# Kernel optimization log

Measured on AMD Instinct MI355X. Metric: run time of the kernel, lower is better.

Reference implementation:

```python
import jax, jax.numpy as jnp
import numpy as np

D_MODEL = 1024
NUM_HEADS = 16
DEPTH = D_MODEL // NUM_HEADS
B, S = 4, 2048


def setup_inputs() -> dict:
    key = jax.random.key(0)
    ks = jax.random.split(key, 11)
    sc = 1.0 / np.sqrt(D_MODEL)
    return {
        "query": jax.random.normal(ks[0], (B, S, D_MODEL), jnp.float32),
        "key_": jax.random.normal(ks[1], (B, S, D_MODEL), jnp.float32),
        "value": jax.random.normal(ks[2], (B, S, D_MODEL), jnp.float32),
        # torch Linear: y = x @ W.T + b, W shape [out, in]
        "Wq": jax.random.normal(ks[3], (D_MODEL, D_MODEL), jnp.float32) * sc,
        "bq": jax.random.normal(ks[4], (D_MODEL,), jnp.float32) * sc,
        "Wk": jax.random.normal(ks[5], (D_MODEL, D_MODEL), jnp.float32) * sc,
        "bk": jax.random.normal(ks[6], (D_MODEL,), jnp.float32) * sc,
        "Wv": jax.random.normal(ks[7], (D_MODEL, D_MODEL), jnp.float32) * sc,
        "bv": jax.random.normal(ks[8], (D_MODEL,), jnp.float32) * sc,
        "Wo": jax.random.normal(ks[9], (D_MODEL, D_MODEL), jnp.float32) * sc,
        "bo": jax.random.normal(ks[10], (D_MODEL,), jnp.float32) * sc,
    }


def _split_heads(x):
    # [B,S,D] -> [B,H,S,depth]
    b, s, _ = x.shape
    return x.reshape(b, s, NUM_HEADS, DEPTH).transpose(0, 2, 1, 3)


def reference(query, key_, value, Wq, bq, Wk, bk, Wv, bv, Wo, bo):
    Q = _split_heads(query @ Wq.T + bq)
    K = _split_heads(key_ @ Wk.T + bk)
    V = _split_heads(value @ Wv.T + bv)
    scale = 1.0 / jnp.sqrt(jnp.float32(DEPTH))
    scores = jnp.einsum("bhqd,bhkd->bhqk", Q, K) * scale  # [B,H,S,S]
    attention_weights = jax.nn.softmax(scores, axis=-1)
    out = jnp.einsum("bhqk,bhkd->bhqd", attention_weights, V)
    out = out.transpose(0, 2, 1, 3).reshape(query.shape[0], -1, D_MODEL)
    out = out @ Wo.T + bo
    return out, attention_weights
```

## Files before the change

kernel.cpp:

```cpp
#include <hip/hip_runtime.h>

#define NHEAD 16
#define SEQ 2048
#define DMODEL 1024
#define BB 4
#define MROWS (BB*SEQ)
#define NBH (BB*NHEAD)
#define NT (SEQ/32)

typedef float f32x4 __attribute__((ext_vector_type(4)));
typedef _Float16 f16x8 __attribute__((ext_vector_type(8)));
typedef _Float16 f16x4 __attribute__((ext_vector_type(4)));

static __device__ __forceinline__ f32x4 mfma16(f16x8 a, f16x8 b, f32x4 c) {
  return __builtin_amdgcn_mfma_f32_16x16x32_f16(a, b, c, 0, 0, 0);
}

static __device__ __forceinline__ void gload_lds16(const unsigned short* g, unsigned short* l) {
  __builtin_amdgcn_global_load_lds(
      (const __attribute__((address_space(1))) unsigned int*)g,
      (__attribute__((address_space(3))) unsigned int*)l, 16, 0, 0);
}

static __device__ __forceinline__ ushort4 cvt4(float4 x) {
  ushort4 h;
  h.x = __builtin_bit_cast(unsigned short, (_Float16)x.x);
  h.y = __builtin_bit_cast(unsigned short, (_Float16)x.y);
  h.z = __builtin_bit_cast(unsigned short, (_Float16)x.z);
  h.w = __builtin_bit_cast(unsigned short, (_Float16)x.w);
  return h;
}

__global__ __launch_bounds__(256)
void round3_f16(const float* __restrict__ q, const float* __restrict__ k,
                const float* __restrict__ v,
                unsigned short* __restrict__ oq, unsigned short* __restrict__ ok,
                unsigned short* __restrict__ ov, int n4)
{
  const float* src = (blockIdx.y == 0) ? q : (blockIdx.y == 1) ? k : v;
  unsigned short* dst = (blockIdx.y == 0) ? oq : (blockIdx.y == 1) ? ok : ov;
  int i = blockIdx.x*256 + threadIdx.x;
  const int stride = gridDim.x*256;
  for (; i < n4; i += stride)
    ((ushort4*)dst)[i] = cvt4(((const float4*)src)[i]);
}

__global__ __launch_bounds__(256)
void round_w4(const float* __restrict__ w0, const float* __restrict__ w1,
              const float* __restrict__ w2, const float* __restrict__ w3,
              unsigned short* __restrict__ o0, unsigned short* __restrict__ o1,
              unsigned short* __restrict__ o2, unsigned short* __restrict__ o3, int n4)
{
  const float* src = (blockIdx.y == 0) ? w0 : (blockIdx.y == 1) ? w1
                   : (blockIdx.y == 2) ? w2 : w3;
  unsigned short* dst = (blockIdx.y == 0) ? o0 : (blockIdx.y == 1) ? o1
                      : (blockIdx.y == 2) ? o2 : o3;
  int i = blockIdx.x*256 + threadIdx.x;
  const int stride = gridDim.x*256;
  for (; i < n4; i += stride)
    ((ushort4*)dst)[i] = cvt4(((const float4*)src)[i]);
}

static __device__ __forceinline__ void stage_proj(
    unsigned short* ab, unsigned short* bb,
    const unsigned short* __restrict__ Xf, const unsigned short* __restrict__ Wf,
    int m0, int n0, int k0, int tid)
{
#pragma unroll
  for (int r = 0; r < 2; ++r) {
    const int gi = r*256 + tid;
    const int row = gi >> 2, c = gi & 3;
    const int lg = c ^ ((row >> 1) & 3);
    gload_lds16(Xf + (size_t)(m0+row)*DMODEL + k0 + lg*8,
                ab + r*2048 + (tid & 0xC0)*8);
  }
#pragma unroll
  for (int r = 0; r < 2; ++r) {
    const int gi = r*256 + tid;
    const int row = gi >> 2, c = gi & 3;
    const int lg = c ^ ((row >> 1) & 3);
    gload_lds16(Wf + (size_t)(n0+row)*DMODEL + k0 + lg*8,
                bb + r*2048 + (tid & 0xC0)*8);
  }
}

template<int MODE>
__global__ __launch_bounds__(256, 2)
void proj_gemm(const unsigned short* __restrict__ Xf, const unsigned short* __restrict__ Wf,
               const float* __restrict__ bias, float oscale,
               unsigned short* __restrict__ o16, float* __restrict__ o_f32)
{
  __shared__ unsigned short As[2][128][32];
  __shared__ unsigned short Bs[2][128][32];
  const int tid  = threadIdx.x;
  const int wid  = tid >> 6, lane = tid & 63;
  const int g    = lane >> 4, r16 = lane & 15;
  const int id   = blockIdx.y*64 + blockIdx.x;
  const int xcd  = id & 7, slot = id >> 3;
  const int m0   = (xcd*8 + (slot & 7)) * 128;
  const int n0   = (slot >> 3) * 128;
  const int wr   = wid >> 1, wc = wid & 1;

  f32x4 acc[4][4] = {};

  stage_proj(&As[0][0][0], &Bs[0][0][0], Xf, Wf, m0, n0, 0, tid);
  asm volatile("s_waitcnt vmcnt(0)" ::: "memory");
  __builtin_amdgcn_s_barrier();

  for (int kt = 0; kt < 32; ++kt) {
    const int cur = kt & 1;
    if (kt < 31)
      stage_proj(&As[cur^1][0][0], &Bs[cur^1][0][0], Xf, Wf, m0, n0, (kt+1)*32, tid);

    const unsigned short (*Asb)[32] = As[cur];
    const unsigned short (*Bsb)[32] = Bs[cur];
    f16x8 a[4], b[4];
#pragma unroll
    for (int t = 0; t < 4; ++t) {
      const int ar = wr*64 + t*16 + r16;
      a[t] = *(const f16x8*)((const char*)&Asb[ar][0] + ((g ^ ((ar >> 1) & 3)) << 4));
      const int br = wc*64 + t*16 + r16;
      b[t] = *(const f16x8*)((const char*)&Bsb[br][0] + ((g ^ ((br >> 1) & 3)) << 4));
    }
    __builtin_amdgcn_s_setprio(1);
#pragma unroll
    for (int mt = 0; mt < 4; ++mt)
#pragma unroll
      for (int nt = 0; nt < 4; ++nt)
        acc[mt][nt] = mfma16(a[mt], b[nt], acc[mt][nt]);
    __builtin_amdgcn_s_setprio(0);

    if (kt < 31) {
      asm volatile("s_waitcnt vmcnt(0)" ::: "memory");
      __builtin_amdgcn_s_barrier();
    }
  }

#pragma unroll
  for (int nt = 0; nt < 4; ++nt) {
    const int n  = n0 + wc*64 + nt*16 + r16;
    const float bn = bias[n];
#pragma unroll
    for (int mt = 0; mt < 4; ++mt) {
      const int mb = m0 + wr*64 + mt*16 + g*4;
      if (MODE == 0) {
#pragma unroll
        for (int j = 0; j < 4; ++j) {
          const int m = mb + j;
          const int bt = m >> 11, s = m & (SEQ-1);
          const int hh = n >> 6,  d = n & 63;
          o16[(((size_t)(bt*NHEAD + hh)*SEQ + s) << 6) + d] =
              __builtin_bit_cast(unsigned short, (_Float16)((acc[mt][nt][j] + bn) * oscale));
        }
      } else if (MODE == 1) {
        const int bt = mb >> 11, sb = mb & (SEQ-1);
        const int hh = n >> 6,  d = n & 63;
        ushort4 v;
        v.x = __builtin_bit_cast(unsigned short, (_Float16)(acc[mt][nt][0] + bn));
        v.y = __builtin_bit_cast(unsigned short, (_Float16)(acc[mt][nt][1] + bn));
        v.z = __builtin_bit_cast(unsigned short, (_Float16)(acc[mt][nt][2] + bn));
        v.w = __builtin_bit_cast(unsigned short, (_Float16)(acc[mt][nt][3] + bn));
        *(ushort4*)(o16 + ((size_t)(bt*NHEAD + hh)*64 + d)*SEQ + sb) = v;
      } else {
#pragma unroll
        for (int j = 0; j < 4; ++j)
          o_f32[(size_t)(mb + j)*DMODEL + n] = acc[mt][nt][j] + bn;
      }
    }
  }
}

static __device__ __forceinline__ void stage_k(unsigned short* dst,
    const unsigned short* __restrict__ Kf, size_t kbase, int k0, int tid)
{
  const int row = tid >> 3, c = tid & 7;
  const int sg = c ^ (row & 7);
  gload_lds16(Kf + kbase + (size_t)(k0+row)*64 + sg*8, dst + (tid & 0xC0)*8);
}

static __device__ __forceinline__ void stage_v(unsigned short* dst,
    const unsigned short* __restrict__ Vtg, int bh, int k0, int tid)
{
  const int row = tid >> 2, c = tid & 3;
  const int lg = c ^ ((row >> 1) & 3);
  gload_lds16(Vtg + ((size_t)bh*64 + row)*SEQ + k0 + lg*8, dst + (tid & 0xC0)*8);
}

__global__ __launch_bounds__(256, 5)
void attn_fused(const unsigned short* __restrict__ Qf, const unsigned short* __restrict__ Kf,
                const unsigned short* __restrict__ Vtg,
                float* __restrict__ wout, unsigned short* __restrict__ of16)
{
  __shared__ unsigned short Ks[3][32][64];
  __shared__ unsigned short Vs[3][64][32];
  __shared__ unsigned short PA[4][16][40];
  const int tid = threadIdx.x, wid = tid >> 6, lane = tid & 63;
  const int g = lane >> 4, r16 = lane & 15;
  const int id = blockIdx.y*32 + blockIdx.x;
  const int xcd = id & 7, slot = id >> 3;
  const int bh = (slot >> 5)*8 + xcd;
  const int bx = slot & 31;
  const int bt = bh >> 4, hh = bh & (NHEAD-1);
  const int s0 = bx*64 + wid*16;
  const size_t kbase = (size_t)bh*SEQ*64;

  const size_t qoff = ((size_t)bh*SEQ + s0 + r16)*64 + (size_t)g*8;
  const f16x8 qh0 = *(const f16x8*)(Qf + qoff);
  const f16x8 qh1 = *(const f16x8*)(Qf + qoff + 32);

  float lp = 0.f;
  stage_k(&Ks[0][0][0], Kf, kbase, 0, tid);
  stage_k(&Ks[1][0][0], Kf, kbase, 32, tid);
  asm volatile("s_waitcnt vmcnt(1)" ::: "memory");
  __builtin_amdgcn_s_barrier();
  {
    int cur = 0, nxt = 2;
    for (int kt = 0; kt < NT; ++kt) {
      const bool pf = kt < NT-2;
      if (pf) stage_k(&Ks[nxt][0][0], Kf, kbase, (kt+2)*32, tid);
#pragma unroll
      for (int sub = 0; sub < 2; ++sub) {
        const int krow = sub*16 + r16;
        const char* pk = (const char*)&Ks[cur][krow][0];
        const int sx = krow & 7;
        const f16x8 kh0 = *(const f16x8*)(pk + (((g    ) ^ sx) << 4));
        const f16x8 kh1 = *(const f16x8*)(pk + (((4 | g) ^ sx) << 4));
        f32x4 acc = {};
        __builtin_amdgcn_s_setprio(1);
        acc = mfma16(kh0, qh0, acc);
        acc = mfma16(kh1, qh1, acc);
        __builtin_amdgcn_s_setprio(0);
#pragma unroll
        for (int j = 0; j < 4; ++j) lp += __builtin_exp2f(acc[j]);
      }
      if (pf) { asm volatile("s_waitcnt vmcnt(1)" ::: "memory"); }
      else    { asm volatile("s_waitcnt vmcnt(0)" ::: "memory"); }
      __builtin_amdgcn_s_barrier();
      cur = (cur == 2) ? 0 : cur + 1;
      nxt = (nxt == 2) ? 0 : nxt + 1;
    }
  }
  lp += __shfl_xor(lp, 16);
  lp += __shfl_xor(lp, 32);
  const float li = 1.0f / lp;

  f32x4 acco[4] = {};
  char* paw = (char*)&PA[wid][0][0];

  stage_k(&Ks[0][0][0], Kf, kbase, 0, tid);
  stage_v(&Vs[0][0][0], Vtg, bh, 0, tid);
  stage_k(&Ks[1][0][0], Kf, kbase, 32, tid);
  stage_v(&Vs[1][0][0], Vtg, bh, 32, tid);
  asm volatile("s_waitcnt vmcnt(2)" ::: "memory");
  __builtin_amdgcn_s_barrier();
  {
    int cur = 0, nxt = 2;
    for (int kt = 0; kt < NT; ++kt) {
      if (kt < NT-2) {
        stage_k(&Ks[nxt][0][0], Kf, kbase, (kt+2)*32, tid);
        stage_v(&Vs[nxt][0][0], Vtg, bh, (kt+2)*32, tid);
      }
#pragma unroll
      for (int sub = 0; sub < 2; ++sub) {
        const int krow = sub*16 + r16;
        const char* pk = (const char*)&Ks[cur][krow][0];
        const int sx = krow & 7;
        const f16x8 kh0 = *(const f16x8*)(pk + (((g    ) ^ sx) << 4));
        const f16x8 kh1 = *(const f16x8*)(pk + (((4 | g) ^ sx) << 4));
        f32x4 acc = {};
        __builtin_amdgcn_s_setprio(1);
        acc = mfma16(kh0, qh0, acc);
        acc = mfma16(kh1, qh1, acc);
        __builtin_amdgcn_s_setprio(0);
        f32x4 w4;
        f16x4 p4;
#pragma unroll
        for (int j = 0; j < 4; ++j) {
          w4[j] = __builtin_exp2f(acc[j]) * li;
          p4[j] = (_Float16)w4[j];
        }
        float* wp = wout + ((size_t)bh*SEQ + s0 + r16)*SEQ + kt*32 + sub*16 + 4*g;
        __builtin_nontemporal_store(w4, (f32x4*)wp);
        *(f16x4*)(paw + r16*80 + ((((2*sub + (g >> 1)) ^ (r16 & 3)) << 4) | ((g & 1) << 3))) = p4;
      }
      asm volatile("s_waitcnt lgkmcnt(0)" ::: "memory");
      const f16x8 pa = *(const f16x8*)(paw + r16*80 + ((g ^ (r16 & 3)) << 4));
      __builtin_amdgcn_s_setprio(1);
#pragma unroll
      for (int nt = 0; nt < 4; ++nt) {
        const int vrow = nt*16 + r16;
        const f16x8 vv = *(const f16x8*)((const char*)&Vs[cur][vrow][0] +
                                         ((g ^ ((vrow >> 1) & 3)) << 4));
        acco[nt] = mfma16(pa, vv, acco[nt]);
      }
      __builtin_amdgcn_s_setprio(0);
      if (kt == 0) {
        asm volatile("s_waitcnt vmcnt(4)" ::: "memory"); __builtin_amdgcn_s_barrier();
      } else if (kt < NT-2) {
        asm volatile("s_waitcnt vmcnt(6)" ::: "memory"); __builtin_amdgcn_s_barrier();
      } else if (kt == NT-2) {
        asm volatile("s_waitcnt vmcnt(4)" ::: "memory"); __builtin_amdgcn_s_barrier();
      }
      cur = (cur == 2) ? 0 : cur + 1;
      nxt = (nxt == 2) ? 0 : nxt + 1;
    }
  }

#pragma unroll
  for (int nt = 0; nt < 4; ++nt)
#pragma unroll
    for (int j = 0; j < 4; ++j)
      of16[((size_t)bt*SEQ + s0 + 4*g + j)*DMODEL + hh*64 + nt*16 + r16] =
          __builtin_bit_cast(unsigned short, (_Float16)acco[nt][j]);
}

extern "C" void kernel_launch(void* const* d_in, const int* in_sizes, int n_in,
                              void* d_out, int out_size, void* d_ws, size_t ws_size,
                              hipStream_t stream)
{
  const float* query = (const float*)d_in[0];
  const float* key_  = (const float*)d_in[1];
  const float* value = (const float*)d_in[2];
  const float* Wq = (const float*)d_in[3];
  const float* bq = (const float*)d_in[4];
  const float* Wk = (const float*)d_in[5];
  const float* bk = (const float*)d_in[6];
  const float* Wv = (const float*)d_in[7];
  const float* bv = (const float*)d_in[8];
  const float* Wo = (const float*)d_in[9];
  const float* bo = (const float*)d_in[10];

  const size_t NE = (size_t)NBH * SEQ * 64;
  const size_t NW = (size_t)DMODEL * DMODEL;
  unsigned short* Xq16 = (unsigned short*)d_ws;
  unsigned short* Xk16 = Xq16 + NE;
  unsigned short* Xv16 = Xk16 + NE;
  unsigned short* Qf   = Xv16 + NE;
  unsigned short* Kf   = Qf + NE;
  unsigned short* Vt   = Kf + NE;
  unsigned short* Wq16 = Vt + NE;
  unsigned short* Wk16 = Wq16 + NW;
  unsigned short* Wv16 = Wk16 + NW;
  unsigned short* Wo16 = Wv16 + NW;
  unsigned short* Of   = Xq16;

  float* out0  = (float*)d_out;
  float* wattn = out0 + (size_t)MROWS * DMODEL;

  const int nX4 = MROWS*DMODEL/4, nW4 = DMODEL*DMODEL/4;
  const float QSCALE = 0.125f * 1.4426950408889634f;
  dim3 gg(64, 8);

  round3_f16<<<dim3(1024, 3), 256, 0, stream>>>(query, key_, value, Xq16, Xk16, Xv16, nX4);
  round_w4<<<dim3(256, 4), 256, 0, stream>>>(Wq, Wk, Wv, Wo, Wq16, Wk16, Wv16, Wo16, nW4);

  proj_gemm<0><<<gg, dim3(256), 0, stream>>>(Xq16, Wq16, bq, QSCALE, Qf, nullptr);
  proj_gemm<0><<<gg, dim3(256), 0, stream>>>(Xk16, Wk16, bk, 1.0f, Kf, nullptr);
  proj_gemm<1><<<gg, dim3(256), 0, stream>>>(Xv16, Wv16, bv, 1.0f, Vt, nullptr);

  attn_fused<<<dim3(32, NBH), dim3(256), 0, stream>>>(Qf, Kf, Vt, wattn, Of);

  proj_gemm<2><<<gg, dim3(256), 0, stream>>>(Of, Wo16, bo, 1.0f, nullptr, out0);
}
```

Baseline: 500.1 us.

## Merge QKV projections into one launch and double query rows per attention wave

The three Q/K/V projection GEMMs are merged into one launch with a z-dimension that selects operands, which removes two kernel launches and lets the three GEMMs share the GPU concurrently. The attention kernel now has each wave handle 32 query rows instead of 16, so each K/V tile loaded into LDS feeds twice as many MFMAs. The grid is halved to match, the P staging buffer is doubled, and the vmcnt waits are adjusted for the extra outstanding stores. In exchange it raises register pressure (launch bounds go from 5 to 4 blocks per SM) and leaves fewer blocks to balance load across the GPU.

```diff
diff --git a/kernel.cpp b/kernel.cpp
--- a/kernel.cpp
+++ b/kernel.cpp
@@ -84,11 +84,102 @@
   }
 }
 
-template<int MODE>
 __global__ __launch_bounds__(256, 2)
-void proj_gemm(const unsigned short* __restrict__ Xf, const unsigned short* __restrict__ Wf,
-               const float* __restrict__ bias, float oscale,
-               unsigned short* __restrict__ o16, float* __restrict__ o_f32)
+void proj_qkv(const unsigned short* __restrict__ Xq, const unsigned short* __restrict__ Xk,
+              const unsigned short* __restrict__ Xv,
+              const unsigned short* __restrict__ Wqm, const unsigned short* __restrict__ Wkm,
+              const unsigned short* __restrict__ Wvm,
+              const float* __restrict__ bq, const float* __restrict__ bk,
+              const float* __restrict__ bv, float qscale,
+              unsigned short* __restrict__ oQ, unsigned short* __restrict__ oK,
+              unsigned short* __restrict__ oV)
+{
+  __shared__ unsigned short As[2][128][32];
+  __shared__ unsigned short Bs[2][128][32];
+  const int z = blockIdx.z;
+  const unsigned short* Xf = (z == 0) ? Xq : (z == 1) ? Xk : Xv;
+  const unsigned short* Wf = (z == 0) ? Wqm : (z == 1) ? Wkm : Wvm;
+  const float* bias = (z == 0) ? bq : (z == 1) ? bk : bv;
+  unsigned short* o16 = (z == 0) ? oQ : (z == 1) ? oK : oV;
+  const float oscale = (z == 0) ? qscale : 1.0f;
+
+  const int tid  = threadIdx.x;
+  const int wid  = tid >> 6, lane = tid & 63;
+  const int g    = lane >> 4, r16 = lane & 15;
+  const int id   = blockIdx.y*64 + blockIdx.x;
+  const int xcd  = id & 7, slot = id >> 3;
+  const int m0   = (xcd*8 + (slot & 7)) * 128;
+  const int n0   = (slot >> 3) * 128;
+  const int wr   = wid >> 1, wc = wid & 1;
+
+  f32x4 acc[4][4] = {};
+
+  stage_proj(&As[0][0][0], &Bs[0][0][0], Xf, Wf, m0, n0, 0, tid);
+  asm volatile("s_waitcnt vmcnt(0)" ::: "memory");
+  __builtin_amdgcn_s_barrier();
+
+  for (int kt = 0; kt < 32; ++kt) {
+    const int cur = kt & 1;
+    if (kt < 31)
+      stage_proj(&As[cur^1][0][0], &Bs[cur^1][0][0], Xf, Wf, m0, n0, (kt+1)*32, tid);
+
+    const unsigned short (*Asb)[32] = As[cur];
+    const unsigned short (*Bsb)[32] = Bs[cur];
+    f16x8 a[4], b[4];
+#pragma unroll
+    for (int t = 0; t < 4; ++t) {
+      const int ar = wr*64 + t*16 + r16;
+      a[t] = *(const f16x8*)((const char*)&Asb[ar][0] + ((g ^ ((ar >> 1) & 3)) << 4));
+      const int br = wc*64 + t*16 + r16;
+      b[t] = *(const f16x8*)((const char*)&Bsb[br][0] + ((g ^ ((br >> 1) & 3)) << 4));
+    }
+    __builtin_amdgcn_s_setprio(1);
+#pragma unroll
+    for (int mt = 0; mt < 4; ++mt)
+#pragma unroll
+      for (int nt = 0; nt < 4; ++nt)
+        acc[mt][nt] = mfma16(a[mt], b[nt], acc[mt][nt]);
+    __builtin_amdgcn_s_setprio(0);
+
+    if (kt < 31) {
+      asm volatile("s_waitcnt vmcnt(0)" ::: "memory");
+      __builtin_amdgcn_s_barrier();
+    }
+  }
+
+#pragma unroll
+  for (int nt = 0; nt < 4; ++nt) {
+    const int n  = n0 + wc*64 + nt*16 + r16;
+    const float bn = bias[n];
+#pragma unroll
+    for (int mt = 0; mt < 4; ++mt) {
+      const int mb = m0 + wr*64 + mt*16 + g*4;
+      if (z < 2) {
+#pragma unroll
+        for (int j = 0; j < 4; ++j) {
+          const int m = mb + j;
+          const int bt = m >> 11, s = m & (SEQ-1);
+          const int hh = n >> 6,  d = n & 63;
+          o16[(((size_t)(bt*NHEAD + hh)*SEQ + s) << 6) + d] =
+              __builtin_bit_cast(unsigned short, (_Float16)((acc[mt][nt][j] + bn) * oscale));
+        }
+      } else {
+        const int bt = mb >> 11, sb = mb & (SEQ-1);
+        const int hh = n >> 6,  d = n & 63;
+        ushort4 v;
+        v.x = __builtin_bit_cast(unsigned short, (_Float16)(acc[mt][nt][0] + bn));
+        v.y = __builtin_bit_cast(unsigned short, (_Float16)(acc[mt][nt][1] + bn));
+        v.z = __builtin_bit_cast(unsigned short, (_Float16)(acc[mt][nt][2] + bn));
+        v.w = __builtin_bit_cast(unsigned short, (_Float16)(acc[mt][nt][3] + bn));
+        *(ushort4*)(o16 + ((size_t)(bt*NHEAD + hh)*64 + d)*SEQ + sb) = v;
+      }
+    }
+  }
+}
+
+__global__ __launch_bounds__(256, 2)
+void proj_o(const unsigned short* __restrict__ Xf, const unsigned short* __restrict__ Wf,
+            const float* __restrict__ bias, float* __restrict__ o_f32)
 {
   __shared__ unsigned short As[2][128][32];
   __shared__ unsigned short Bs[2][128][32];
@@ -143,29 +234,9 @@
 #pragma unroll
     for (int mt = 0; mt < 4; ++mt) {
       const int mb = m0 + wr*64 + mt*16 + g*4;
-      if (MODE == 0) {
-#pragma unroll
-        for (int j = 0; j < 4; ++j) {
-          const int m = mb + j;
-          const int bt = m >> 11, s = m & (SEQ-1);
-          const int hh = n >> 6,  d = n & 63;
-          o16[(((size_t)(bt*NHEAD + hh)*SEQ + s) << 6) + d] =
-              __builtin_bit_cast(unsigned short, (_Float16)((acc[mt][nt][j] + bn) * oscale));
-        }
-      } else if (MODE == 1) {
-        const int bt = mb >> 11, sb = mb & (SEQ-1);
-        const int hh = n >> 6,  d = n & 63;
-        ushort4 v;
-        v.x = __builtin_bit_cast(unsigned short, (_Float16)(acc[mt][nt][0] + bn));
-        v.y = __builtin_bit_cast(unsigned short, (_Float16)(acc[mt][nt][1] + bn));
-        v.z = __builtin_bit_cast(unsigned short, (_Float16)(acc[mt][nt][2] + bn));
-        v.w = __builtin_bit_cast(unsigned short, (_Float16)(acc[mt][nt][3] + bn));
-        *(ushort4*)(o16 + ((size_t)(bt*NHEAD + hh)*64 + d)*SEQ + sb) = v;
-      } else {
-#pragma unroll
-        for (int j = 0; j < 4; ++j)
-          o_f32[(size_t)(mb + j)*DMODEL + n] = acc[mt][nt][j] + bn;
-      }
+#pragma unroll
+      for (int j = 0; j < 4; ++j)
+        o_f32[(size_t)(mb + j)*DMODEL + n] = acc[mt][nt][j] + bn;
     }
   }
 }
@@ -186,29 +257,31 @@
   gload_lds16(Vtg + ((size_t)bh*64 + row)*SEQ + k0 + lg*8, dst + (tid & 0xC0)*8);
 }
 
-__global__ __launch_bounds__(256, 5)
+__global__ __launch_bounds__(256, 4)
 void attn_fused(const unsigned short* __restrict__ Qf, const unsigned short* __restrict__ Kf,
                 const unsigned short* __restrict__ Vtg,
                 float* __restrict__ wout, unsigned short* __restrict__ of16)
 {
   __shared__ unsigned short Ks[3][32][64];
   __shared__ unsigned short Vs[3][64][32];
-  __shared__ unsigned short PA[4][16][40];
+  __shared__ unsigned short PA[4][32][40];
   const int tid = threadIdx.x, wid = tid >> 6, lane = tid & 63;
   const int g = lane >> 4, r16 = lane & 15;
-  const int id = blockIdx.y*32 + blockIdx.x;
+  const int id = blockIdx.y*16 + blockIdx.x;
   const int xcd = id & 7, slot = id >> 3;
-  const int bh = (slot >> 5)*8 + xcd;
-  const int bx = slot & 31;
+  const int bh = (slot >> 4)*8 + xcd;
+  const int bx = slot & 15;
   const int bt = bh >> 4, hh = bh & (NHEAD-1);
-  const int s0 = bx*64 + wid*16;
+  const int s0 = bx*128 + wid*32;
   const size_t kbase = (size_t)bh*SEQ*64;
 
-  const size_t qoff = ((size_t)bh*SEQ + s0 + r16)*64 + (size_t)g*8;
-  const f16x8 qh0 = *(const f16x8*)(Qf + qoff);
-  const f16x8 qh1 = *(const f16x8*)(Qf + qoff + 32);
-
-  float lp = 0.f;
+  const size_t qoffA = ((size_t)bh*SEQ + s0 + r16)*64 + (size_t)g*8;
+  const f16x8 qA0 = *(const f16x8*)(Qf + qoffA);
+  const f16x8 qA1 = *(const f16x8*)(Qf + qoffA + 32);
+  const f16x8 qB0 = *(const f16x8*)(Qf + qoffA + 16*64);
+  const f16x8 qB1 = *(const f16x8*)(Qf + qoffA + 16*64 + 32);
+
+  float lpA = 0.f, lpB = 0.f;
   stage_k(&Ks[0][0][0], Kf, kbase, 0, tid);
   stage_k(&Ks[1][0][0], Kf, kbase, 32, tid);
   asm volatile("s_waitcnt vmcnt(1)" ::: "memory");
@@ -225,13 +298,16 @@
         const int sx = krow & 7;
         const f16x8 kh0 = *(const f16x8*)(pk + (((g    ) ^ sx) << 4));
         const f16x8 kh1 = *(const f16x8*)(pk + (((4 | g) ^ sx) << 4));
-        f32x4 acc = {};
+        f32x4 aA = {}, aB = {};
         __builtin_amdgcn_s_setprio(1);
-        acc = mfma16(kh0, qh0, acc);
-        acc = mfma16(kh1, qh1, acc);
+        aA = mfma16(kh0, qA0, aA); aA = mfma16(kh1, qA1, aA);
+        aB = mfma16(kh0, qB0, aB); aB = mfma16(kh1, qB1, aB);
         __builtin_amdgcn_s_setprio(0);
 #pragma unroll
-        for (int j = 0; j < 4; ++j) lp += __builtin_exp2f(acc[j]);
+        for (int j = 0; j < 4; ++j) {
+          lpA += __builtin_exp2f(aA[j]);
+          lpB += __builtin_exp2f(aB[j]);
+        }
       }
       if (pf) { asm volatile("s_waitcnt vmcnt(1)" ::: "memory"); }
       else    { asm volatile("s_waitcnt vmcnt(0)" ::: "memory"); }
@@ -240,11 +316,12 @@
       nxt = (nxt == 2) ? 0 : nxt + 1;
     }
   }
-  lp += __shfl_xor(lp, 16);
-  lp += __shfl_xor(lp, 32);
-  const float li = 1.0f / lp;
-
-  f32x4 acco[4] = {};
+  lpA += __shfl_xor(lpA, 16); lpA += __shfl_xor(lpA, 32);
+  lpB += __shfl_xor(lpB, 16); lpB += __shfl_xor(lpB, 32);
+  const float liA = 1.0f / lpA;
+  const float liB = 1.0f / lpB;
+
+  f32x4 accoA[4] = {}, accoB[4] = {};
   char* paw = (char*)&PA[wid][0][0];
 
   stage_k(&Ks[0][0][0], Kf, kbase, 0, tid);
@@ -267,39 +344,48 @@
         const int sx = krow & 7;
         const f16x8 kh0 = *(const f16x8*)(pk + (((g    ) ^ sx) << 4));
         const f16x8 kh1 = *(const f16x8*)(pk + (((4 | g) ^ sx) << 4));
-        f32x4 acc = {};
+        f32x4 aA = {}, aB = {};
         __builtin_amdgcn_s_setprio(1);
-        acc = mfma16(kh0, qh0, acc);
-        acc = mfma16(kh1, qh1, acc);
+        aA = mfma16(kh0, qA0, aA); aA = mfma16(kh1, qA1, aA);
+        aB = mfma16(kh0, qB0, aB); aB = mfma16(kh1, qB1, aB);
         __builtin_amdgcn_s_setprio(0);
-        f32x4 w4;
-        f16x4 p4;
-#pragma unroll
-        for (int j = 0; j < 4; ++j) {
-          w4[j] = __builtin_exp2f(acc[j]) * li;
-          p4[j] = (_Float16)w4[j];
+        const int pacol = ((((2*sub + (g >> 1)) ^ (r16 & 3)) << 4) | ((g & 1) << 3));
+        {
+          f32x4 w4; f16x4 p4;
+#pragma unroll
+          for (int j = 0; j < 4; ++j) { w4[j] = __builtin_exp2f(aA[j]) * liA; p4[j] = (_Float16)w4[j]; }
+          float* wp = wout + ((size_t)bh*SEQ + s0 + r16)*SEQ + kt*32 + sub*16 + 4*g;
+          __builtin_nontemporal_store(w4, (f32x4*)wp);
+          *(f16x4*)(paw + r16*80 + pacol) = p4;
         }
-        float* wp = wout + ((size_t)bh*SEQ + s0 + r16)*SEQ + kt*32 + sub*16 + 4*g;
-        __builtin_nontemporal_store(w4, (f32x4*)wp);
-        *(f16x4*)(paw + r16*80 + ((((2*sub + (g >> 1)) ^ (r16 & 3)) << 4) | ((g & 1) << 3))) = p4;
+        {
+          f32x4 w4; f16x4 p4;
+#pragma unroll
+          for (int j = 0; j < 4; ++j) { w4[j] = __builtin_exp2f(aB[j]) * liB; p4[j] = (_Float16)w4[j]; }
+          float* wp = wout + ((size_t)bh*SEQ + s0 + 16 + r16)*SEQ + kt*32 + sub*16 + 4*g;
+          __builtin_nontemporal_store(w4, (f32x4*)wp);
+          *(f16x4*)(paw + (16 + r16)*80 + pacol) = p4;
+        }
       }
       asm volatile("s_waitcnt lgkmcnt(0)" ::: "memory");
-      const f16x8 pa = *(const f16x8*)(paw + r16*80 + ((g ^ (r16 & 3)) << 4));
+      const f16x8 paA = *(const f16x8*)(paw + r16*80 + ((g ^ (r16 & 3)) << 4));
+      const f16x8 paB = *(const f16x8*)(paw + (16 + r16)*80 + ((g ^ (r16 & 3)) << 4));
       __builtin_amdgcn_s_setprio(1);
 #pragma unroll
       for (int nt = 0; nt < 4; ++nt) {
         const int vrow = nt*16 + r16;
         const f16x8 vv = *(const f16x8*)((const char*)&Vs[cur][vrow][0] +
                                          ((g ^ ((vrow >> 1) & 3)) << 4));
-        acco[nt] = mfma16(pa, vv, acco[nt]);
+        accoA[nt] = mfma16(paA, vv, accoA[nt]);
+        accoB[nt] = mfma16(paB, vv, accoB[nt]);
       }
       __builtin_amdgcn_s_setprio(0);
       if (kt == 0) {
-        asm volatile("s_waitcnt vmcnt(4)" ::: "memory"); __builtin_amdgcn_s_barrier();
+        asm volatile("s_waitcnt vmcnt(6)" ::: "memory"); __builtin_amdgcn_s_barrier();
       } else if (kt < NT-2) {
-        asm volatile("s_waitcnt vmcnt(6)" ::: "memory"); __builtin_amdgcn_s_barrier();
+        asm volatile("s_waitcnt vmcnt(10)" ::: "memory"); __builtin_amdgcn_s_barrier();
       } else if (kt == NT-2) {
-        asm volatile("s_waitcnt vmcnt(4)" ::: "memory"); __builtin_amdgcn_s_barrier();
+        asm volatile("s_waitcnt vmcnt(8)" ::: "memory"); __builtin_amdgcn_s_barrier();
       }
       cur = (cur == 2) ? 0 : cur + 1;
       nxt = (nxt == 2) ? 0 : nxt + 1;
@@ -309,9 +395,12 @@
 #pragma unroll
   for (int nt = 0; nt < 4; ++nt)
 #pragma unroll
-    for (int j = 0; j < 4; ++j)
+    for (int j = 0; j < 4; ++j) {
       of16[((size_t)bt*SEQ + s0 + 4*g + j)*DMODEL + hh*64 + nt*16 + r16] =
-          __builtin_bit_cast(unsigned short, (_Float16)acco[nt][j]);
+          __builtin_bit_cast(unsigned short, (_Float16)accoA[nt][j]);
+      of16[((size_t)bt*SEQ + s0 + 16 + 4*g + j)*DMODEL + hh*64 + nt*16 + r16] =
+          __builtin_bit_cast(unsigned short, (_Float16)accoB[nt][j]);
+    }
 }
 
 extern "C" void kernel_launch(void* const* d_in, const int* in_sizes, int n_in,
@@ -354,11 +443,10 @@
   round3_f16<<<dim3(1024, 3), 256, 0, stream>>>(query, key_, value, Xq16, Xk16, Xv16, nX4);
   round_w4<<<dim3(256, 4), 256, 0, stream>>>(Wq, Wk, Wv, Wo, Wq16, Wk16, Wv16, Wo16, nW4);
 
-  proj_gemm<0><<<gg, dim3(256), 0, stream>>>(Xq16, Wq16, bq, QSCALE, Qf, nullptr);
-  proj_gemm<0><<<gg, dim3(256), 0, stream>>>(Xk16, Wk16, bk, 1.0f, Kf, nullptr);
-  proj_gemm<1><<<gg, dim3(256), 0, stream>>>(Xv16, Wv16, bv, 1.0f, Vt, nullptr);
-
-  attn_fused<<<dim3(32, NBH), dim3(256), 0, stream>>>(Qf, Kf, Vt, wattn, Of);
-
-  proj_gemm<2><<<gg, dim3(256), 0, stream>>>(Of, Wo16, bo, 1.0f, nullptr, out0);
-}
+  proj_qkv<<<dim3(64, 8, 3), dim3(256), 0, stream>>>(
+      Xq16, Xk16, Xv16, Wq16, Wk16, Wv16, bq, bk, bv, QSCALE, Qf, Kf, Vt);
+
+  attn_fused<<<dim3(16, NBH), dim3(256), 0, stream>>>(Qf, Kf, Vt, wattn, Of);
+
+  proj_o<<<gg, dim3(256), 0, stream>>>(Of, Wo16, bo, out0);
+}
```

Result: slower. 540.5 us (+8.1%).
